# Kernel tuning notes

Measured on AMD Instinct MI355X. Metric: run time of the kernel, lower is better.

The kernel has to match this reference:

```python
import jax, jax.numpy as jnp
import numpy as np

EMBED_DIM = 768
N_HEADS = 12
HEAD_DIM = EMBED_DIM // N_HEADS
SCALE = HEAD_DIM ** 0.5


def setup_inputs() -> dict:
    key = jax.random.key(0)
    k1, k2, k3 = jax.random.split(key, 3)
    x = jax.random.normal(k1, (2, 2048, EMBED_DIM), dtype=jnp.float32)
    # weights stored [in, out] so forward is x @ W (equivalent to torch Linear with W.T)
    w_qkv = jax.random.normal(k2, (EMBED_DIM, 3 * EMBED_DIM), dtype=jnp.float32) * (EMBED_DIM ** -0.5)
    w_proj = jax.random.normal(k3, (EMBED_DIM, EMBED_DIM), dtype=jnp.float32) * (EMBED_DIM ** -0.5)
    return {"x": x, "w_qkv": w_qkv, "w_proj": w_proj}


def reference(x, w_qkv, w_proj):
    B, N, C = x.shape
    qkv = x @ w_qkv  # [B, N, 3C]
    qkv = qkv.reshape(B, N, 3, N_HEADS, HEAD_DIM)
    qkv = jnp.transpose(qkv, (2, 0, 3, 1, 4))  # [3, B, H, N, hd]
    q, k, v = qkv[0], qkv[1], qkv[2]
    attn = jnp.einsum("bhnd,bhmd->bhnm", q, k) / SCALE  # [B, H, N, N]
    attn = jax.nn.softmax(attn, axis=-1)
    out = jnp.einsum("bhnm,bhmd->bhnd", attn, v)  # [B, H, N, hd]
    out = jnp.transpose(out, (0, 2, 1, 3)).reshape(B, N, C)
    return out @ w_proj
```

## Files before the change

### kernel.cpp

```cpp
#include <hip/hip_runtime.h>
#include <hip/hip_bf16.h>
#include <stdint.h>

typedef uint16_t u16;
typedef __attribute__((ext_vector_type(4))) float f32x4;
typedef __attribute__((ext_vector_type(8))) short bf16x8;

#define LOG2E 1.4426950408889634f

static __device__ __forceinline__ u16 f2b(float x){
  union { float f; uint32_t u; } a; a.f = x;
  uint32_t r = a.u + 0x7FFFu + ((a.u >> 16) & 1u);
  return (u16)(r >> 16);
}

static __device__ __forceinline__ uint32_t pkrhu(float lo, float hi){
  union { float f; uint32_t u; } a, b; a.f = lo; b.f = hi;
  return __builtin_amdgcn_perm(b.u + 0x8000u, a.u + 0x8000u, 0x07060302u);
}

#define GLD16(g, l) __builtin_amdgcn_global_load_lds((const __attribute__((address_space(1))) void*)(g), (__attribute__((address_space(3))) void*)(l), 16, 0, 0)

__global__ __launch_bounds__(256) void k_prep(const float* __restrict__ x, u16* __restrict__ Xb,
                                              const float* __restrict__ wqkv, u16* __restrict__ WqkvT,
                                              const float* __restrict__ wproj, u16* __restrict__ WprojT){
  __shared__ float t[32][33];
  const int bid = blockIdx.x, tid = threadIdx.x;
  if (bid < 1536){
    int i = bid * 256 + tid;
    const f32x4* p = (const f32x4*)(x + (size_t)i * 8);
    f32x4 a = p[0], b = p[1];
    u16 h[8];
#pragma unroll
    for (int j = 0; j < 4; ++j){ h[j] = f2b(a[j]); h[4+j] = f2b(b[j]); }
    *(bf16x8*)(Xb + (size_t)i * 8) = *(const bf16x8*)h;
    return;
  }
  const float* in; u16* out; int R, C, bx, by;
  if (bid < 1536 + 1728){
    int q = bid - 1536; in = wqkv; out = WqkvT; R = 768; C = 2304; bx = q % 72; by = q / 72;
  } else {
    int q = bid - 1536 - 1728; in = wproj; out = WprojT; R = 768; C = 768; bx = q % 24; by = q / 24;
  }
  int c0 = bx * 32, r0 = by * 32;
  int tx = tid & 31, ty = tid >> 5;
#pragma unroll
  for (int i = 0; i < 32; i += 8) t[ty + i][tx] = in[(size_t)(r0 + ty + i) * C + c0 + tx];
  __syncthreads();
#pragma unroll
  for (int i = 0; i < 32; i += 8) out[(size_t)(c0 + ty + i) * R + r0 + tx] = f2b(t[tx][ty + i]);
}

__global__ __launch_bounds__(256) void k_gemmqkv(const u16* __restrict__ A, const u16* __restrict__ Bt,
                                                 u16* __restrict__ Qp, u16* __restrict__ Kp, u16* __restrict__ Vtp){
  __shared__ __align__(16) u16 SM[14336];
  u16* Al = SM; u16* Bl = SM + 8192;
  const int tid = threadIdx.x;
  const int w = tid >> 6, l = tid & 63;
  const int m0 = blockIdx.x * 128, n0 = blockIdx.y * 96;
  const int wm = (w >> 1) * 64, wn = (w & 1) * 48;
  const int lg = l >> 4, lr = l & 15;
  f32x4 acc[4][3] = {};
  const u16* asrc = A  + (size_t)(m0 + w*32 + (l >> 3)) * 768 + (l & 7) * 8;
  const u16* bsrc = Bt + (size_t)(n0 + w*24 + (l >> 3)) * 768 + (l & 7) * 8;
  for (int k0 = 0; k0 < 768; k0 += 64){
#pragma unroll
    for (int i = 0; i < 4; ++i)
      GLD16(asrc + (size_t)(i*8)*768 + k0, &Al[(w*32 + i*8) * 64]);
#pragma unroll
    for (int i = 0; i < 3; ++i)
      GLD16(bsrc + (size_t)(i*8)*768 + k0, &Bl[(w*24 + i*8) * 64]);
    __syncthreads();
    bf16x8 af[4][2], bfr[3][2];
#pragma unroll
    for (int mf = 0; mf < 4; ++mf)
#pragma unroll
      for (int ks = 0; ks < 2; ++ks)
        af[mf][ks] = *(const bf16x8*)&Al[(wm + mf*16 + lr) * 64 + ks*32 + lg*8];
#pragma unroll
    for (int nf = 0; nf < 3; ++nf)
#pragma unroll
      for (int ks = 0; ks < 2; ++ks)
        bfr[nf][ks] = *(const bf16x8*)&Bl[(wn + nf*16 + lr) * 64 + ks*32 + lg*8];
#pragma unroll
    for (int ks = 0; ks < 2; ++ks)
#pragma unroll
      for (int mf = 0; mf < 4; ++mf)
#pragma unroll
        for (int nf = 0; nf < 3; ++nf)
          acc[mf][nf] = __builtin_amdgcn_mfma_f32_16x16x32_bf16(af[mf][ks], bfr[nf][ks], acc[mf][nf], 0, 0, 0);
    __syncthreads();
  }

  const int which = n0 / 768;
  const int nl0 = n0 - which * 768;
  if (which < 2){
    u16* dst = (which == 0) ? Qp : Kp;
    const float sc = (which == 0) ? 0.125f * LOG2E : 1.0f;
#pragma unroll
    for (int mf = 0; mf < 4; ++mf)
#pragma unroll
      for (int nf = 0; nf < 3; ++nf)
#pragma unroll
        for (int r = 0; r < 4; ++r){
          int m = m0 + wm + mf*16 + lg*4 + r;
          int n = nl0 + wn + nf*16 + lr;
          int b = m >> 11, row = m & 2047, hh = n >> 6, d = n & 63;
          dst[(size_t)((b*12 + hh)*2048 + row) * 64 + d] = f2b(acc[mf][nf][r] * sc);
        }
  } else {
#pragma unroll
    for (int mf = 0; mf < 4; ++mf)
#pragma unroll
      for (int nf = 0; nf < 3; ++nf)
#pragma unroll
        for (int r = 0; r < 4; ++r){
          int mrow = wm + mf*16 + lg*4 + r;
          int c    = wn + nf*16 + lr;
          SM[c * 128 + mrow] = f2b(acc[mf][nf][r]);
        }
    __syncthreads();
#pragma unroll
    for (int rr = 0; rr < 6; ++rr){
      int c  = rr*16 + (tid >> 4);
      int mo = (tid & 15) * 8;
      bf16x8 v = *(const bf16x8*)&SM[c * 128 + mo];
      int n = nl0 + c, hh = n >> 6, d = n & 63;
      int m = m0 + mo, b = m >> 11, key = m & 2047;
      *(bf16x8*)&Vtp[(size_t)((b*12 + hh)*64 + d) * 2048 + key] = v;
    }
  }
}

__global__ __launch_bounds__(256) void k_gemm64(const u16* __restrict__ A, const u16* __restrict__ Bt,
                                                float* __restrict__ Co){
  __shared__ __align__(16) u16 SM[8192];
  u16* Al = SM; u16* Bl = SM + 4096;
  const int tid = threadIdx.x;
  const int w = tid >> 6, l = tid & 63;
  const int m0 = blockIdx.x * 64, n0 = blockIdx.y * 64;
  const int wm = (w >> 1) * 32, wn = (w & 1) * 32;
  const int lg = l >> 4, lr = l & 15;
  f32x4 acc[2][2] = {};
  const u16* asrc = A  + (size_t)(m0 + w*16 + (l >> 3)) * 768 + (l & 7) * 8;
  const u16* bsrc = Bt + (size_t)(n0 + w*16 + (l >> 3)) * 768 + (l & 7) * 8;
  for (int k0 = 0; k0 < 768; k0 += 64){
#pragma unroll
    for (int i = 0; i < 2; ++i){
      GLD16(asrc + (size_t)(i*8)*768 + k0, &Al[(w*16 + i*8) * 64]);
      GLD16(bsrc + (size_t)(i*8)*768 + k0, &Bl[(w*16 + i*8) * 64]);
    }
    __syncthreads();
    bf16x8 af[2][2], bfr[2][2];
#pragma unroll
    for (int mf = 0; mf < 2; ++mf)
#pragma unroll
      for (int ks = 0; ks < 2; ++ks){
        af[mf][ks]  = *(const bf16x8*)&Al[(wm + mf*16 + lr) * 64 + ks*32 + lg*8];
        bfr[mf][ks] = *(const bf16x8*)&Bl[(wn + mf*16 + lr) * 64 + ks*32 + lg*8];
      }
#pragma unroll
    for (int ks = 0; ks < 2; ++ks)
#pragma unroll
      for (int mf = 0; mf < 2; ++mf)
#pragma unroll
        for (int nf = 0; nf < 2; ++nf)
          acc[mf][nf] = __builtin_amdgcn_mfma_f32_16x16x32_bf16(af[mf][ks], bfr[nf][ks], acc[mf][nf], 0, 0, 0);
    __syncthreads();
  }
#pragma unroll
  for (int mf = 0; mf < 2; ++mf)
#pragma unroll
    for (int nf = 0; nf < 2; ++nf)
#pragma unroll
      for (int r = 0; r < 4; ++r)
        Co[(size_t)(m0 + wm + mf*16 + lg*4 + r) * 768 + n0 + wn + nf*16 + lr] = acc[mf][nf][r];
}

__global__ __launch_bounds__(512, 3) void k_attn(const u16* __restrict__ Qp, const u16* __restrict__ Kp,
                                                 const u16* __restrict__ Vtp, u16* __restrict__ AO){
  __shared__ __align__(16) u16 SM[24576];
  const int tid = threadIdx.x, w = tid >> 6, l = tid & 63;
  const int QH = w >> 1, KH = w & 1;
  const int lg = l >> 4, lr = l & 15;
  const int qt_b = blockIdx.x, bh = blockIdx.y;
  const int b = bh / 12, hh = bh - b * 12;
  const size_t base = (size_t)bh * (2048 * 64);
  const u16* Qg = Qp + base; const u16* Kg = Kp + base; const u16* Vg = Vtp + base;
  const int q0w = qt_b * 64 + QH * 16;
  const int rsw = (lr & 7) * 8;

  bf16x8 qf[2];
#pragma unroll
  for (int ks = 0; ks < 2; ++ks)
    qf[ks] = *(const bf16x8*)&Qg[(size_t)(q0w + lr) * 64 + ks*32 + lg*8];

  f32x4 oacc[4] = {};
  float lp = 0.f;

  const int p_  = tid >> 3;
  const int sk  = 32*(p_ >> 5) + 8*((p_ >> 2) & 3) + 4*((p_ >> 4) & 1) + (p_ & 3);
  const int cs8 = (((tid & 7) ^ (p_ & 7)) << 3);
  const u16* kp = Kg + (size_t)sk * 64 + cs8;
  const u16* vp = Vg + ((size_t)p_ << 11) + cs8;
  const int drow = p_ * 64;
  u16* const K0 = SM + 0     + drow;  u16* const V0 = SM + 12288 + drow;
  u16* const K1 = SM + 4096  + drow;  u16* const V1 = SM + 16384 + drow;
  u16* const K2 = SM + 8192  + drow;  u16* const V2 = SM + 20480 + drow;

  auto compute = [&](const u16* Kc, const u16* Vc){
    f32x4 s[2] = {};
    bf16x8 kfr[2][2];
#pragma unroll
    for (int kf = 0; kf < 2; ++kf)
#pragma unroll
      for (int ks = 0; ks < 2; ++ks)
        kfr[kf][ks] = *(const bf16x8*)&Kc[(KH*32 + kf*16 + lr) * 64 + ((ks*32 + lg*8) ^ rsw)];
    __builtin_amdgcn_s_setprio(1);
#pragma unroll
    for (int ks = 0; ks < 2; ++ks)
#pragma unroll
      for (int kf = 0; kf < 2; ++kf)
        s[kf] = __builtin_amdgcn_mfma_f32_16x16x32_bf16(kfr[kf][ks], qf[ks], s[kf], 0, 0, 0);
    __builtin_amdgcn_s_setprio(0);

    float p00 = __builtin_exp2f(s[0][0]);
    float p01 = __builtin_exp2f(s[0][1]);
    float p02 = __builtin_exp2f(s[0][2]);
    float p03 = __builtin_exp2f(s[0][3]);
    float p10 = __builtin_exp2f(s[1][0]);
    float p11 = __builtin_exp2f(s[1][1]);
    float p12 = __builtin_exp2f(s[1][2]);
    float p13 = __builtin_exp2f(s[1][3]);
    lp += ((p00 + p01) + (p02 + p03)) + ((p10 + p11) + (p12 + p13));
    union { uint32_t u[4]; bf16x8 v; } fr;
    fr.u[0] = pkrhu(p00, p01);
    fr.u[1] = pkrhu(p02, p03);
    fr.u[2] = pkrhu(p10, p11);
    fr.u[3] = pkrhu(p12, p13);

    bf16x8 vfr[4];
#pragma unroll
    for (int nf = 0; nf < 4; ++nf)
      vfr[nf] = *(const bf16x8*)&Vc[(nf*16 + lr) * 64 + ((KH*32 + lg*8) ^ rsw)];
    __builtin_amdgcn_s_setprio(1);
#pragma unroll
    for (int nf = 0; nf < 4; ++nf)
      oacc[nf] = __builtin_amdgcn_mfma_f32_16x16x32_bf16(vfr[nf], fr.v, oacc[nf], 0, 0, 0);
    __builtin_amdgcn_s_setprio(0);
  };

#define STAGE2(KD, VD) do { GLD16(kp, KD); GLD16(vp, VD); kp += 4096; vp += 64; } while(0)
#define BAR_CNT2  do { asm volatile("s_waitcnt vmcnt(2)" ::: "memory"); \
                       __builtin_amdgcn_s_barrier(); __builtin_amdgcn_sched_barrier(0); } while(0)
#define BAR_CNT0  do { asm volatile("s_waitcnt vmcnt(0)" ::: "memory"); \
                       __builtin_amdgcn_s_barrier(); __builtin_amdgcn_sched_barrier(0); } while(0)

  STAGE2(K0, V0);
  STAGE2(K1, V1);
  BAR_CNT2;

  for (int g = 0; g < 10; ++g){
    STAGE2(K2, V2);  compute(SM + 0,    SM + 12288);  BAR_CNT2;
    STAGE2(K0, V0);  compute(SM + 4096, SM + 16384);  BAR_CNT2;
    STAGE2(K1, V1);  compute(SM + 8192, SM + 20480);  BAR_CNT2;
  }
  compute(SM + 0,    SM + 12288);
  BAR_CNT0;
  compute(SM + 4096, SM + 16384);

#undef STAGE2
#undef BAR_CNT2
#undef BAR_CNT0

  float lt = lp;
  lt += __shfl_xor(lt, 16);
  lt += __shfl_xor(lt, 32);

  __syncthreads();
  float* Osc = (float*)SM;
  float* Lsc = Osc + 64 * 65;
  if (KH == 1){
#pragma unroll
    for (int nf = 0; nf < 4; ++nf)
#pragma unroll
      for (int r = 0; r < 4; ++r)
        Osc[(QH*16 + lr) * 65 + nf*16 + lg*4 + r] = oacc[nf][r];
    if (lg == 0) Lsc[QH*16 + lr] = lt;
  }
  __syncthreads();
  if (KH == 0){
    float inv = 1.0f / (lt + Lsc[QH*16 + lr]);
#pragma unroll
    for (int nf = 0; nf < 4; ++nf)
#pragma unroll
      for (int r = 0; r < 4; ++r){
        float o = oacc[nf][r] + Osc[(QH*16 + lr) * 65 + nf*16 + lg*4 + r];
        AO[(size_t)((b << 11) + q0w + lr) * 768 + hh*64 + nf*16 + lg*4 + r] = f2b(o * inv);
      }
  }
}

extern "C" void kernel_launch(void* const* d_in, const int* in_sizes, int n_in,
                              void* d_out, int out_size, void* d_ws, size_t ws_size,
                              hipStream_t stream){
  const float* x      = (const float*)d_in[0];
  const float* w_qkv  = (const float*)d_in[1];
  const float* w_proj = (const float*)d_in[2];
  float* out = (float*)d_out;
  char* ws = (char*)d_ws;
  u16* Xb     = (u16*)(ws + 0);
  u16* WqkvT  = (u16*)(ws + 6291456);
  u16* WprojT = (u16*)(ws + 9830400);
  u16* Qp     = (u16*)(ws + 11010048);
  u16* Kp     = (u16*)(ws + 17301504);
  u16* Vtp    = (u16*)(ws + 23592960);
  u16* AO     = (u16*)(ws + 29884416);

  k_prep<<<3840, 256, 0, stream>>>(x, Xb, w_qkv, WqkvT, w_proj, WprojT);
  k_gemmqkv<<<dim3(32, 24), 256, 0, stream>>>(Xb, WqkvT, Qp, Kp, Vtp);
  k_attn<<<dim3(32, 24), 512, 0, stream>>>(Qp, Kp, Vtp, AO);
  k_gemm64<<<dim3(64, 12), 256, 0, stream>>>(AO, WprojT, out);
}
```

Before: 88.27 us.

## Double-buffer QKV GEMM LDS tiles with XOR-swizzled layout

The QKV projection GEMM main loop moves from a single-buffered 64-wide K tile to two 32-wide K stages that alternate. The next stage's global-to-LDS loads are issued while MFMAs consume the current one. The LDS layout is XOR-swizzled on the 16-byte octet index to cut bank conflicts on fragment reads. This hides global load latency behind compute, at the cost of twice as many barriers per unit of K.

```diff
diff --git a/kernel.cpp b/kernel.cpp
--- a/kernel.cpp
+++ b/kernel.cpp
@@ -54,43 +54,59 @@
 __global__ __launch_bounds__(256) void k_gemmqkv(const u16* __restrict__ A, const u16* __restrict__ Bt,
                                                  u16* __restrict__ Qp, u16* __restrict__ Kp, u16* __restrict__ Vtp){
   __shared__ __align__(16) u16 SM[14336];
-  u16* Al = SM; u16* Bl = SM + 8192;
   const int tid = threadIdx.x;
   const int w = tid >> 6, l = tid & 63;
   const int m0 = blockIdx.x * 128, n0 = blockIdx.y * 96;
   const int wm = (w >> 1) * 64, wn = (w & 1) * 48;
   const int lg = l >> 4, lr = l & 15;
   f32x4 acc[4][3] = {};
-  const u16* asrc = A  + (size_t)(m0 + w*32 + (l >> 3)) * 768 + (l & 7) * 8;
-  const u16* bsrc = Bt + (size_t)(n0 + w*24 + (l >> 3)) * 768 + (l & 7) * 8;
-  for (int k0 = 0; k0 < 768; k0 += 64){
-#pragma unroll
-    for (int i = 0; i < 4; ++i)
-      GLD16(asrc + (size_t)(i*8)*768 + k0, &Al[(w*32 + i*8) * 64]);
-#pragma unroll
-    for (int i = 0; i < 3; ++i)
-      GLD16(bsrc + (size_t)(i*8)*768 + k0, &Bl[(w*24 + i*8) * 64]);
-    __syncthreads();
-    bf16x8 af[4][2], bfr[3][2];
-#pragma unroll
-    for (int mf = 0; mf < 4; ++mf)
-#pragma unroll
-      for (int ks = 0; ks < 2; ++ks)
-        af[mf][ks] = *(const bf16x8*)&Al[(wm + mf*16 + lr) * 64 + ks*32 + lg*8];
-#pragma unroll
-    for (int nf = 0; nf < 3; ++nf)
-#pragma unroll
-      for (int ks = 0; ks < 2; ++ks)
-        bfr[nf][ks] = *(const bf16x8*)&Bl[(wn + nf*16 + lr) * 64 + ks*32 + lg*8];
-#pragma unroll
-    for (int ks = 0; ks < 2; ++ks)
-#pragma unroll
-      for (int mf = 0; mf < 4; ++mf)
-#pragma unroll
-        for (int nf = 0; nf < 3; ++nf)
-          acc[mf][nf] = __builtin_amdgcn_mfma_f32_16x16x32_bf16(af[mf][ks], bfr[nf][ks], acc[mf][nf], 0, 0, 0);
-    __syncthreads();
-  }
+
+  const int tr = tid >> 2;
+  const int soct = ((tid & 3) ^ (tr & 3)) * 8;
+  const u16* a0 = A  + (size_t)(m0 + tr) * 768 + soct;
+  const u16* a1 = A  + (size_t)(m0 + 64 + tr) * 768 + soct;
+  const u16* b0 = Bt + (size_t)(n0 + tr) * 768 + soct;
+  const u16* b1 = Bt + (size_t)(n0 + 64 + tr) * 768 + soct;
+  u16* const A0d = SM + 0     + tid*8;  u16* const A0e = SM + 2048  + tid*8;
+  u16* const A1d = SM + 4096  + tid*8;  u16* const A1e = SM + 6144  + tid*8;
+  u16* const B0d = SM + 8192  + tid*8;  u16* const B0e = SM + 10240 + tid*8;
+  u16* const B1d = SM + 11264 + tid*8;  u16* const B1e = SM + 13312 + tid*8;
+
+#define QSTAGE0 do { GLD16(a0, A0d); GLD16(a1, A0e); GLD16(b0, B0d); if (tid < 128) GLD16(b1, B0e); \
+                     a0 += 32; a1 += 32; b0 += 32; b1 += 32; } while(0)
+#define QSTAGE1 do { GLD16(a0, A1d); GLD16(a1, A1e); GLD16(b0, B1d); if (tid < 128) GLD16(b1, B1e); \
+                     a0 += 32; a1 += 32; b0 += 32; b1 += 32; } while(0)
+
+  const int foct = (lg ^ (lr & 3)) * 8;
+
+#define QCOMP(ABASE, BBASE) do {                                                            \
+    bf16x8 af[4], bfr[3];                                                                   \
+    _Pragma("unroll")                                                                       \
+    for (int mf = 0; mf < 4; ++mf)                                                          \
+      af[mf] = *(const bf16x8*)&SM[(ABASE) + (wm + mf*16 + lr) * 32 + foct];                \
+    _Pragma("unroll")                                                                       \
+    for (int nf = 0; nf < 3; ++nf)                                                          \
+      bfr[nf] = *(const bf16x8*)&SM[(BBASE) + (wn + nf*16 + lr) * 32 + foct];               \
+    _Pragma("unroll")                                                                       \
+    for (int mf = 0; mf < 4; ++mf)                                                          \
+      _Pragma("unroll")                                                                     \
+      for (int nf = 0; nf < 3; ++nf)                                                        \
+        acc[mf][nf] = __builtin_amdgcn_mfma_f32_16x16x32_bf16(af[mf], bfr[nf], acc[mf][nf], 0, 0, 0); \
+  } while(0)
+
+  QSTAGE0;
+  __syncthreads();
+  for (int i = 0; i < 12; ++i){
+    QSTAGE1;
+    QCOMP(0, 8192);
+    __syncthreads();
+    if (i < 11) QSTAGE0;
+    QCOMP(4096, 11264);
+    __syncthreads();
+  }
+#undef QSTAGE0
+#undef QSTAGE1
+#undef QCOMP
 
   const int which = n0 / 768;
   const int nl0 = n0 - which * 768;
```

After: 87.34 us. Within noise of the previous version (-1.1%).
